# Kernel optimization log

Measured on AMD Instinct MI355X. Metric: run time of the kernel, lower is better.

## Reference

```python
import jax, jax.numpy as jnp
import numpy as np

N_NODES = 50000
N_EDGES = 800000
IN_DIM = 128
EDGE_DIM = 16
HIDDEN = 128
N_LAYERS = 3
N_GRAPHS = 256
BN_EPS = 1e-5


def setup_inputs() -> dict:
    key = jax.random.key(0)
    ks = jax.random.split(key, 24)
    s = 0.05
    inp = {
        "x": jax.random.normal(ks[0], (N_NODES, IN_DIM), jnp.float32),
        "edge_index": jax.random.randint(ks[1], (2, N_EDGES), 0, N_NODES, jnp.int32),
        "edge_attr": jax.random.normal(ks[2], (N_EDGES, EDGE_DIM), jnp.float32),
        "batch": jnp.sort(jax.random.randint(ks[3], (N_NODES,), 0, N_GRAPHS, jnp.int32)),
        "n_graphs": N_GRAPHS,
        # input projection
        "lin_in_w": jax.random.normal(ks[4], (IN_DIM, HIDDEN), jnp.float32) * s,
        "lin_in_b": jnp.zeros((HIDDEN,), jnp.float32),
        # per-layer message MLP (stacked over layers)
        "msg_w1": jax.random.normal(ks[5], (N_LAYERS, HIDDEN + EDGE_DIM, HIDDEN), jnp.float32) * s,
        "msg_b1": jnp.zeros((N_LAYERS, HIDDEN), jnp.float32),
        "msg_w2": jax.random.normal(ks[6], (N_LAYERS, HIDDEN, HIDDEN), jnp.float32) * s,
        "msg_b2": jnp.zeros((N_LAYERS, HIDDEN), jnp.float32),
        # BatchNorm (eval mode: running stats)
        "bn_gamma": jnp.ones((N_LAYERS, HIDDEN), jnp.float32),
        "bn_beta": jnp.zeros((N_LAYERS, HIDDEN), jnp.float32),
        "bn_mean": jax.random.normal(ks[7], (N_LAYERS, HIDDEN), jnp.float32) * 0.01,
        "bn_var": jax.random.uniform(ks[8], (N_LAYERS, HIDDEN), jnp.float32, 0.5, 1.5),
        # GRUCell params (PyTorch layout: [3*H, H], gate order r,z,n)
        "gru_wih": jax.random.normal(ks[9], (N_LAYERS, 3 * HIDDEN, HIDDEN), jnp.float32) * s,
        "gru_whh": jax.random.normal(ks[10], (N_LAYERS, 3 * HIDDEN, HIDDEN), jnp.float32) * s,
        "gru_bih": jnp.zeros((N_LAYERS, 3 * HIDDEN), jnp.float32),
        "gru_bhh": jnp.zeros((N_LAYERS, 3 * HIDDEN), jnp.float32),
        # readout linear: [2H -> H]
        "ro_w": jax.random.normal(ks[11], (2 * HIDDEN, HIDDEN), jnp.float32) * s,
        "ro_b": jnp.zeros((HIDDEN,), jnp.float32),
    }
    return inp


def _gru_cell(x, h, wih, whh, bih, bhh):
    gi = x @ wih.T + bih  # [N, 3H]
    gh = h @ whh.T + bhh
    ir, iz, inn = jnp.split(gi, 3, axis=1)
    hr, hz, hn = jnp.split(gh, 3, axis=1)
    r = jax.nn.sigmoid(ir + hr)
    z = jax.nn.sigmoid(iz + hz)
    n = jnp.tanh(inn + r * hn)
    return (1.0 - z) * n + z * h


def reference(x, edge_index, edge_attr, batch, n_graphs,
              lin_in_w, lin_in_b, msg_w1, msg_b1, msg_w2, msg_b2,
              bn_gamma, bn_beta, bn_mean, bn_var,
              gru_wih, gru_whh, gru_bih, gru_bhh, ro_w, ro_b):
    h = jax.nn.relu(x @ lin_in_w + lin_in_b)  # [N, H]
    src, dst = edge_index[0], edge_index[1]
    n_nodes = h.shape[0]
    for l in range(N_LAYERS):
        m_in = jnp.concatenate([h[src], edge_attr], axis=1)  # [E, H+Ed]
        m = jax.nn.relu(m_in @ msg_w1[l] + msg_b1[l]) @ msg_w2[l] + msg_b2[l]  # [E, H]
        agg = jax.ops.segment_sum(m, dst, num_segments=n_nodes)  # scatter-add
        h_new = _gru_cell(agg, h, gru_wih[l], gru_whh[l], gru_bih[l], gru_bhh[l])
        bn = (h_new - bn_mean[l]) * jax.lax.rsqrt(bn_var[l] + BN_EPS) * bn_gamma[l] + bn_beta[l]
        h = h + bn  # dropout is identity in eval mode
    # readout: segment mean + segment max over graphs
    cnt = jax.ops.segment_sum(jnp.ones((n_nodes, 1), h.dtype), batch, num_segments=n_graphs)
    z_sum = jax.ops.segment_sum(h, batch, num_segments=n_graphs)
    z_mean = z_sum / jnp.maximum(cnt, 1.0)
    z_max = jax.ops.segment_max(h, batch, num_segments=n_graphs)
    z_max = jnp.where(cnt > 0, z_max, 0.0)  # empty graphs -> 0 (as in torch code)
    z = jax.nn.relu(jnp.concatenate([z_mean, z_max], axis=1) @ ro_w + ro_b)
    return z
```

## Files before the change

kernel.cpp:

```cpp
#include <hip/hip_runtime.h>
#include <math.h>

constexpr int NN = 50000;
constexpr int NE = 800000;
constexpr int H  = 128;
constexpr int ED = 16;
constexpr int NL = 3;
constexpr int NG = 256;

typedef __attribute__((ext_vector_type(8))) short bf8;
typedef __attribute__((ext_vector_type(4))) float f32x4;

__device__ __forceinline__ unsigned short f2bf(float f) {
    unsigned u = __float_as_uint(f);
    unsigned r = (u + 0x7FFFu + ((u >> 16) & 1u)) >> 16;
    return (unsigned short)r;
}
__device__ __forceinline__ float bf2f(unsigned short b) {
    return __uint_as_float(((unsigned)b) << 16);
}

__global__ __launch_bounds__(256) void k_sort_zero(int* __restrict__ counts) {
    int i = blockIdx.x * 256 + threadIdx.x;
    counts[i] = 0;
}

__global__ __launch_bounds__(256) void k_hist(const int* __restrict__ ei,
                                              int* __restrict__ counts) {
    int e = blockIdx.x * 256 + threadIdx.x;
    if (e < NE) atomicAdd(&counts[ei[NE + e]], 1);
}

__global__ __launch_bounds__(256) void k_scan1(const int* __restrict__ counts,
                                               int* __restrict__ incl,
                                               int* __restrict__ bsum) {
    __shared__ int s[256];
    int t = threadIdx.x;
    int i = blockIdx.x * 256 + t;
    int v = counts[i];
    s[t] = v;
    __syncthreads();
    #pragma unroll
    for (int off = 1; off < 256; off <<= 1) {
        int x = (t >= off) ? s[t - off] : 0;
        __syncthreads();
        s[t] += x;
        __syncthreads();
    }
    incl[i] = s[t];
    if (t == 255) bsum[blockIdx.x] = s[255];
}

__global__ __launch_bounds__(256) void k_scan2(int* __restrict__ bsum) {
    __shared__ int s[256];
    int t = threadIdx.x;
    int v = (t < 196) ? bsum[t] : 0;
    s[t] = v;
    __syncthreads();
    #pragma unroll
    for (int off = 1; off < 256; off <<= 1) {
        int x = (t >= off) ? s[t - off] : 0;
        __syncthreads();
        s[t] += x;
        __syncthreads();
    }
    if (t < 196) bsum[t] = s[t] - v;
}

__global__ __launch_bounds__(256) void k_scan3(const int* __restrict__ counts,
                                               const int* __restrict__ incl,
                                               const int* __restrict__ bsum,
                                               int* __restrict__ cur) {
    int i = blockIdx.x * 256 + threadIdx.x;
    cur[i] = incl[i] - counts[i] + bsum[blockIdx.x];
}

__global__ __launch_bounds__(256) void k_scatter_perm(const int* __restrict__ ei,
                                                      int* __restrict__ cur,
                                                      int* __restrict__ perm) {
    int e = blockIdx.x * 256 + threadIdx.x;
    if (e < NE) {
        int d = ei[NE + e];
        int pos = atomicAdd(&cur[d], 1);
        perm[pos] = e;
    }
}

__global__ __launch_bounds__(256) void k_gather(const int* __restrict__ ei,
                                                const float* __restrict__ ea,
                                                int* __restrict__ perm,
                                                int* __restrict__ dsts,
                                                unsigned short* __restrict__ ea_bf) {
    int i = blockIdx.x * 256 + threadIdx.x;
    if (i >= NE) return;
    int e = perm[i];
    perm[i] = ei[e];
    dsts[i] = ei[NE + e];
    const float4* s = (const float4*)(ea + (size_t)e * ED);
    float4 v[4];
    #pragma unroll
    for (int j = 0; j < 4; ++j) v[j] = s[j];
    union { uint4 u[2]; unsigned short sh[16]; } pk;
    #pragma unroll
    for (int j = 0; j < 4; ++j) {
        pk.sh[j * 4 + 0] = f2bf(v[j].x); pk.sh[j * 4 + 1] = f2bf(v[j].y);
        pk.sh[j * 4 + 2] = f2bf(v[j].z); pk.sh[j * 4 + 3] = f2bf(v[j].w);
    }
    uint4* d = (uint4*)(ea_bf + (size_t)i * 16);
    d[0] = pk.u[0];
    d[1] = pk.u[1];
}

__global__ __launch_bounds__(256) void k_prep(const float* __restrict__ wih,
                                              const float* __restrict__ whh,
                                              const float* __restrict__ w1,
                                              const float* __restrict__ w2,
                                              const float* __restrict__ lin_w,
                                              unsigned short* __restrict__ wgru,
                                              unsigned short* __restrict__ w1et,
                                              unsigned short* __restrict__ w2t,
                                              unsigned short* __restrict__ w1ht,
                                              unsigned short* __restrict__ winT) {
    int i = blockIdx.x * 256 + threadIdx.x;
    if (i < 294912) {
        int m = i / 147456, rem = i % 147456;
        wgru[i] = f2bf((m == 0 ? wih : whh)[rem]);
        return;
    }
    i -= 294912;
    if (i < NL * 128 * 32) {
        int l = i / 4096, rem = i % 4096;
        int n = rem >> 5, k = rem & 31;
        float v = (k < ED) ? w1[(size_t)l * 144 * 128 + (size_t)(128 + k) * 128 + n] : 0.f;
        w1et[i] = f2bf(v);
        return;
    }
    i -= NL * 128 * 32;
    if (i < NL * 128 * 128) {
        int l = i / 16384, rem = i % 16384;
        int n = rem >> 7, k = rem & 127;
        w2t[i] = f2bf(w2[(size_t)l * 16384 + (size_t)k * 128 + n]);
        return;
    }
    i -= NL * 128 * 128;
    if (i < NL * 128 * 128) {
        int l = i / 16384, rem = i % 16384;
        int n = rem >> 7, k = rem & 127;
        w1ht[i] = f2bf(w1[(size_t)l * 144 * 128 + (size_t)k * 128 + n]);
        return;
    }
    i -= NL * 128 * 128;
    if (i < 128 * 128) {
        int n = i >> 7, k = i & 127;
        winT[i] = f2bf(lin_w[k * 128 + n]);
    }
}

template <bool RELU, bool BIAS, bool OUT_F32, bool OUT_BF>
__global__ __launch_bounds__(256) void k_mfma_gemm(const float* __restrict__ A,
                                                   const unsigned short* __restrict__ Bt,
                                                   const float* __restrict__ bias,
                                                   float* __restrict__ C_f,
                                                   unsigned short* __restrict__ C_bf,
                                                   int M) {
    __shared__ unsigned short As[32][136];
    const int t = threadIdx.x;
    const int w = t >> 6, lane = t & 63, l15 = lane & 15, q = lane >> 4;
    const int n0 = blockIdx.x * 32;

    bf8 bfr[2][4];
    #pragma unroll
    for (int nt = 0; nt < 2; ++nt) {
        int n = w * 32 + nt * 16 + l15;
        #pragma unroll
        for (int ks = 0; ks < 4; ++ks)
            bfr[nt][ks] = *(const bf8*)(Bt + (size_t)n * 128 + ks * 32 + q * 8);
    }

    {
        int r = t >> 3, cs = (t & 7) * 16;
        int row = n0 + r;
        float4 v[4];
        if (row < M) {
            const float4* src = (const float4*)(A + (size_t)row * H + cs);
            #pragma unroll
            for (int j = 0; j < 4; ++j) v[j] = src[j];
        } else {
            #pragma unroll
            for (int j = 0; j < 4; ++j) v[j] = make_float4(0.f, 0.f, 0.f, 0.f);
        }
        union { uint4 u[2]; unsigned short s[16]; } pk;
        #pragma unroll
        for (int j = 0; j < 4; ++j) {
            pk.s[j * 4 + 0] = f2bf(v[j].x); pk.s[j * 4 + 1] = f2bf(v[j].y);
            pk.s[j * 4 + 2] = f2bf(v[j].z); pk.s[j * 4 + 3] = f2bf(v[j].w);
        }
        *(uint4*)&As[r][cs] = pk.u[0];
        *(uint4*)&As[r][cs + 8] = pk.u[1];
    }
    __syncthreads();

    f32x4 acc[2][2];
    #pragma unroll
    for (int mt = 0; mt < 2; ++mt)
        #pragma unroll
        for (int nt = 0; nt < 2; ++nt) acc[mt][nt] = {0.f, 0.f, 0.f, 0.f};

    #pragma unroll
    for (int ks = 0; ks < 4; ++ks) {
        #pragma unroll
        for (int mt = 0; mt < 2; ++mt) {
            bf8 af = *(const bf8*)&As[mt * 16 + l15][ks * 32 + q * 8];
            acc[mt][0] = __builtin_amdgcn_mfma_f32_16x16x32_bf16(af, bfr[0][ks], acc[mt][0], 0, 0, 0);
            acc[mt][1] = __builtin_amdgcn_mfma_f32_16x16x32_bf16(af, bfr[1][ks], acc[mt][1], 0, 0, 0);
        }
    }

    #pragma unroll
    for (int nt = 0; nt < 2; ++nt) {
        int col = w * 32 + nt * 16 + l15;
        float bv = BIAS ? bias[col] : 0.f;
        #pragma unroll
        for (int mt = 0; mt < 2; ++mt) {
            #pragma unroll
            for (int r = 0; r < 4; ++r) {
                int node = n0 + mt * 16 + q * 4 + r;
                if (node < M) {
                    float v = acc[mt][nt][r] + bv;
                    if (RELU) v = fmaxf(v, 0.f);
                    if (OUT_F32) C_f[(size_t)node * H + col] = v;
                    if (OUT_BF)  C_bf[(size_t)node * H + col] = f2bf(v);
                }
            }
        }
    }
}

__global__ __launch_bounds__(256, 6) void k_edge_mfma(
        const unsigned short* __restrict__ p,
        const int* __restrict__ srcs,
        const int* __restrict__ dsts,
        const unsigned short* __restrict__ ea_bf,
        const unsigned short* __restrict__ w1et,
        const float* __restrict__ b1,
        const unsigned short* __restrict__ w2t,
        const float* __restrict__ b2,
        float* __restrict__ agg) {
    __shared__ unsigned short u_s[64][136];
    __shared__ int src_s[64], dst_s[64];

    const int t    = threadIdx.x;
    const int w    = t >> 6;
    const int lane = t & 63;
    const int l15  = lane & 15;
    const int q    = lane >> 4;

    bf8 w1f[2];
    bf8 w2f[2][4];
    float b1v[2], b2v[2];
    #pragma unroll
    for (int nt = 0; nt < 2; ++nt) {
        int n = w * 32 + nt * 16 + l15;
        w1f[nt] = *(const bf8*)(w1et + (size_t)n * 32 + q * 8);
        #pragma unroll
        for (int ks = 0; ks < 4; ++ks)
            w2f[nt][ks] = *(const bf8*)(w2t + (size_t)n * 128 + ks * 32 + q * 8);
        b1v[nt] = b1[n];
        b2v[nt] = b2[n];
    }

    const f32x4 zero = {0.f, 0.f, 0.f, 0.f};

    for (int base = blockIdx.x * 64; base < NE; base += gridDim.x * 64) {
        if (t < 64)       src_s[t] = srcs[base + t];
        else if (t < 128) dst_s[t - 64] = dsts[base + t - 64];
        __syncthreads();

        {
            int row = t >> 4, seg = t & 15;
            #pragma unroll
            for (int it = 0; it < 4; ++it) {
                int rr = row + 16 * it;
                *(uint4*)&u_s[rr][seg * 8] =
                    *(const uint4*)(p + (size_t)src_s[rr] * H + seg * 8);
            }
        }

        f32x4 acc1[4][2];
        #pragma unroll
        for (int mt = 0; mt < 4; ++mt) {
            bf8 af = {0, 0, 0, 0, 0, 0, 0, 0};
            if (q < 2)
                af = *(const bf8*)(ea_bf + (size_t)(base + mt * 16 + l15) * 16 + q * 8);
            #pragma unroll
            for (int nt = 0; nt < 2; ++nt)
                acc1[mt][nt] = __builtin_amdgcn_mfma_f32_16x16x32_bf16(af, w1f[nt], zero, 0, 0, 0);
        }
        __syncthreads();

        #pragma unroll
        for (int mt = 0; mt < 4; ++mt) {
            #pragma unroll
            for (int r = 0; r < 4; ++r) {
                int er = mt * 16 + q * 4 + r;
                #pragma unroll
                for (int nt = 0; nt < 2; ++nt) {
                    int col = w * 32 + nt * 16 + l15;
                    float v = acc1[mt][nt][r] + bf2f(u_s[er][col]) + b1v[nt];
                    u_s[er][col] = f2bf(fmaxf(v, 0.f));
                }
            }
        }
        __syncthreads();

        f32x4 acc2[4][2];
        #pragma unroll
        for (int mt = 0; mt < 4; ++mt)
            #pragma unroll
            for (int nt = 0; nt < 2; ++nt) acc2[mt][nt] = zero;

        #pragma unroll
        for (int ks = 0; ks < 4; ++ks) {
            #pragma unroll
            for (int mt = 0; mt < 4; ++mt) {
                bf8 af = *(const bf8*)&u_s[mt * 16 + l15][ks * 32 + q * 8];
                acc2[mt][0] = __builtin_amdgcn_mfma_f32_16x16x32_bf16(af, w2f[0][ks], acc2[mt][0], 0, 0, 0);
                acc2[mt][1] = __builtin_amdgcn_mfma_f32_16x16x32_bf16(af, w2f[1][ks], acc2[mt][1], 0, 0, 0);
            }
        }
        __syncthreads();

        #pragma unroll
        for (int mt = 0; mt < 4; ++mt) {
            #pragma unroll
            for (int r = 0; r < 4; ++r) {
                int er = mt * 16 + q * 4 + r;
                #pragma unroll
                for (int nt = 0; nt < 2; ++nt) {
                    int col = w * 32 + nt * 16 + l15;
                    u_s[er][col] = f2bf(acc2[mt][nt][r] + b2v[nt]);
                }
            }
        }
        __syncthreads();

        {
            int c = t & 127, hh = t >> 7;
            float sum = 0.f;
            int prev = dst_s[hh * 32];
            #pragma unroll 4
            for (int i = 0; i < 32; ++i) {
                int e = hh * 32 + i;
                int d = dst_s[e];
                float v = bf2f(u_s[e][c]);
                if (d != prev) {
                    atomicAdd(&agg[(size_t)prev * H + c], sum);
                    sum = 0.f;
                    prev = d;
                }
                sum += v;
            }
            atomicAdd(&agg[(size_t)prev * H + c], sum);
        }
        __syncthreads();
    }
}

__device__ __forceinline__ float sigmoidf_(float x) { return 1.f / (1.f + expf(-x)); }

__global__ __launch_bounds__(256) void k_gru_mfma(const float* __restrict__ agg,
                                                  float* __restrict__ h,
                                                  const unsigned short* __restrict__ wih,
                                                  const unsigned short* __restrict__ whh,
                                                  const float* __restrict__ bih,
                                                  const float* __restrict__ bhh,
                                                  const float* __restrict__ gamma,
                                                  const float* __restrict__ beta,
                                                  const float* __restrict__ mean,
                                                  const float* __restrict__ var) {
    __shared__ unsigned short ab[32][136];
    __shared__ unsigned short hb[32][136];
    __shared__ float hf[32][132];
    const int t = threadIdx.x;
    const int w = t >> 6, lane = t & 63, l15 = lane & 15, q = lane >> 4;
    const int n0 = blockIdx.x * 32;

    {
        int r = t >> 3, cs = (t & 7) * 16;
        int row = n0 + r;
        float4 va[4], vh[4];
        if (row < NN) {
            const float4* sa = (const float4*)(agg + (size_t)row * H + cs);
            const float4* sh = (const float4*)(h + (size_t)row * H + cs);
            #pragma unroll
            for (int j = 0; j < 4; ++j) { va[j] = sa[j]; vh[j] = sh[j]; }
        } else {
            #pragma unroll
            for (int j = 0; j < 4; ++j) {
                va[j] = make_float4(0.f, 0.f, 0.f, 0.f);
                vh[j] = va[j];
            }
        }
        union { uint4 u[2]; unsigned short s[16]; } pa, ph;
        #pragma unroll
        for (int j = 0; j < 4; ++j) {
            pa.s[j * 4 + 0] = f2bf(va[j].x); pa.s[j * 4 + 1] = f2bf(va[j].y);
            pa.s[j * 4 + 2] = f2bf(va[j].z); pa.s[j * 4 + 3] = f2bf(va[j].w);
            ph.s[j * 4 + 0] = f2bf(vh[j].x); ph.s[j * 4 + 1] = f2bf(vh[j].y);
            ph.s[j * 4 + 2] = f2bf(vh[j].z); ph.s[j * 4 + 3] = f2bf(vh[j].w);
            *(float4*)&hf[r][cs + j * 4] = vh[j];
        }
        *(uint4*)&ab[r][cs] = pa.u[0];  *(uint4*)&ab[r][cs + 8] = pa.u[1];
        *(uint4*)&hb[r][cs] = ph.u[0];  *(uint4*)&hb[r][cs + 8] = ph.u[1];
    }
    __syncthreads();

    f32x4 acc[2][2][3][2];
    #pragma unroll
    for (int mt = 0; mt < 2; ++mt)
        #pragma unroll
        for (int io = 0; io < 2; ++io)
            #pragma unroll
            for (int g = 0; g < 3; ++g)
                #pragma unroll
                for (int nt = 0; nt < 2; ++nt) acc[mt][io][g][nt] = {0.f, 0.f, 0.f, 0.f};

    #pragma unroll
    for (int ks = 0; ks < 4; ++ks) {
        bf8 a_a[2], a_h[2];
        #pragma unroll
        for (int mt = 0; mt < 2; ++mt) {
            a_a[mt] = *(const bf8*)&ab[mt * 16 + l15][ks * 32 + q * 8];
            a_h[mt] = *(const bf8*)&hb[mt * 16 + l15][ks * 32 + q * 8];
        }
        #pragma unroll
        for (int g = 0; g < 3; ++g) {
            #pragma unroll
            for (int nt = 0; nt < 2; ++nt) {
                int n = g * 128 + w * 32 + nt * 16 + l15;
                bf8 bi = *(const bf8*)(wih + (size_t)n * 128 + ks * 32 + q * 8);
                bf8 bh = *(const bf8*)(whh + (size_t)n * 128 + ks * 32 + q * 8);
                #pragma unroll
                for (int mt = 0; mt < 2; ++mt) {
                    acc[mt][0][g][nt] = __builtin_amdgcn_mfma_f32_16x16x32_bf16(a_a[mt], bi, acc[mt][0][g][nt], 0, 0, 0);
                    acc[mt][1][g][nt] = __builtin_amdgcn_mfma_f32_16x16x32_bf16(a_h[mt], bh, acc[mt][1][g][nt], 0, 0, 0);
                }
            }
        }
    }

    #pragma unroll
    for (int nt = 0; nt < 2; ++nt) {
        int col = w * 32 + nt * 16 + l15;
        float bir = bih[col], biz = bih[128 + col], bin = bih[256 + col];
        float bhr = bhh[col], bhz = bhh[128 + col], bhn = bhh[256 + col];
        float ga = gamma[col], be = beta[col], mu = mean[col];
        float iv = rsqrtf(var[col] + 1e-5f);
        #pragma unroll
        for (int mt = 0; mt < 2; ++mt) {
            #pragma unroll
            for (int r = 0; r < 4; ++r) {
                int nl = mt * 16 + q * 4 + r;
                int node = n0 + nl;
                if (node < NN) {
                    float ir = acc[mt][0][0][nt][r] + bir;
                    float iz = acc[mt][0][1][nt][r] + biz;
                    float in = acc[mt][0][2][nt][r] + bin;
                    float hr = acc[mt][1][0][nt][r] + bhr;
                    float hz = acc[mt][1][1][nt][r] + bhz;
                    float hn = acc[mt][1][2][nt][r] + bhn;
                    float rg = sigmoidf_(ir + hr);
                    float zg = sigmoidf_(iz + hz);
                    float ng = tanhf(in + rg * hn);
                    float hv = hf[nl][col];
                    float hnew = (1.f - zg) * ng + zg * hv;
                    float bn = (hnew - mu) * iv * ga + be;
                    h[(size_t)node * H + col] = hv + bn;
                }
            }
        }
    }
}

__device__ __forceinline__ unsigned fkey(float f) {
    unsigned b = __float_as_uint(f);
    return (b & 0x80000000u) ? ~b : (b | 0x80000000u);
}
__device__ __forceinline__ float funkey(unsigned k) {
    unsigned b = (k & 0x80000000u) ? (k & 0x7FFFFFFFu) : ~k;
    return __uint_as_float(b);
}

__global__ __launch_bounds__(256) void k_ro_scan(const float* __restrict__ h,
                                                 const int* __restrict__ batch,
                                                 float* __restrict__ gsum,
                                                 unsigned* __restrict__ gmaxb,
                                                 float* __restrict__ gcnt) {
    __shared__ int bt_s[64];
    const int t = threadIdx.x;
    const int n0 = blockIdx.x * 64;
    if (t < 64) bt_s[t] = (n0 + t < NN) ? batch[n0 + t] : -1;
    __syncthreads();

    int c = t & 127, hh = t >> 7;
    float sum = 0.f, mx = -3.4e38f, cnt = 0.f;
    int prev = bt_s[hh * 32];
    #pragma unroll 4
    for (int i = 0; i < 32; ++i) {
        int e = hh * 32 + i;
        int g = bt_s[e];
        if (g != prev) {
            if (prev >= 0) {
                atomicAdd(&gsum[prev * H + c], sum);
                atomicMax(&gmaxb[prev * H + c], fkey(mx));
                if (c == 0) atomicAdd(&gcnt[prev], cnt);
            }
            sum = 0.f; mx = -3.4e38f; cnt = 0.f;
            prev = g;
        }
        if (g >= 0) {
            float v = h[(size_t)(n0 + e) * H + c];
            sum += v;
            mx = fmaxf(mx, v);
            cnt += 1.f;
        }
    }
    if (prev >= 0) {
        atomicAdd(&gsum[prev * H + c], sum);
        atomicMax(&gmaxb[prev * H + c], fkey(mx));
        if (c == 0) atomicAdd(&gcnt[prev], cnt);
    }
}

__global__ __launch_bounds__(128) void k_ro_final(const float* __restrict__ gsum,
                                                  const unsigned* __restrict__ gmaxb,
                                                  const float* __restrict__ gcnt,
                                                  const float* __restrict__ row,
                                                  const float* __restrict__ rob,
                                                  float* __restrict__ out) {
    __shared__ float cat[256];
    const int g = blockIdx.x, t = threadIdx.x;
    float cnt = gcnt[g];
    float inv = 1.f / fmaxf(cnt, 1.f);
    cat[t] = gsum[g * H + t] * inv;
    float mx = funkey(gmaxb[g * H + t]);
    cat[128 + t] = (cnt > 0.f) ? mx : 0.f;
    __syncthreads();
    float acc = rob[t];
    #pragma unroll 4
    for (int k = 0; k < 256; ++k) acc += cat[k] * row[k * H + t];
    out[g * H + t] = fmaxf(acc, 0.f);
}

extern "C" void kernel_launch(void* const* d_in, const int* in_sizes, int n_in,
                              void* d_out, int out_size, void* d_ws, size_t ws_size,
                              hipStream_t stream) {
    const float* x        = (const float*)d_in[0];
    const int*   ei       = (const int*)d_in[1];
    const float* ea       = (const float*)d_in[2];
    const int*   batch    = (const int*)d_in[3];
    const float* lin_in_w = (const float*)d_in[5];
    const float* lin_in_b = (const float*)d_in[6];
    const float* msg_w1   = (const float*)d_in[7];
    const float* msg_b1   = (const float*)d_in[8];
    const float* msg_w2   = (const float*)d_in[9];
    const float* msg_b2   = (const float*)d_in[10];
    const float* bn_gamma = (const float*)d_in[11];
    const float* bn_beta  = (const float*)d_in[12];
    const float* bn_mean  = (const float*)d_in[13];
    const float* bn_var   = (const float*)d_in[14];
    const float* gru_wih  = (const float*)d_in[15];
    const float* gru_whh  = (const float*)d_in[16];
    const float* gru_bih  = (const float*)d_in[17];
    const float* gru_bhh  = (const float*)d_in[18];
    const float* ro_w     = (const float*)d_in[19];
    const float* ro_b     = (const float*)d_in[20];

    float* ws = (float*)d_ws;
    float*          h     = ws;
    float*          agg   = ws + 6400000;
    unsigned short* p_bf  = (unsigned short*)(ws + 12800000);
    float*          gsum  = ws + 16000000;
    unsigned*       gmaxb = (unsigned*)(ws + 16032768);
    float*          gcnt  = ws + 16065536;
    unsigned short* wgru  = (unsigned short*)(ws + 16065792);
    unsigned short* w1et  = (unsigned short*)(ws + 16213248);
    unsigned short* w2t   = (unsigned short*)(ws + 16219392);
    unsigned short* w1ht  = (unsigned short*)(ws + 16243968);
    unsigned short* winT  = (unsigned short*)(ws + 16268544);
    int*            cnts  = (int*)(ws + 16276736);
    int*            incl  = (int*)(ws + 16326912);
    int*            cur   = (int*)(ws + 16377088);
    int*            bsum  = (int*)(ws + 16427264);
    int*            srcs  = (int*)(ws + 16427520);
    int*            dsts  = (int*)(ws + 17227520);
    unsigned short* ea_bf = (unsigned short*)(ws + 18027520);

    k_prep<<<1648, 256, 0, stream>>>(gru_wih, gru_whh, msg_w1, msg_w2, lin_in_w,
                                     wgru, w1et, w2t, w1ht, winT);

    k_sort_zero<<<196, 256, 0, stream>>>(cnts);
    k_hist<<<3125, 256, 0, stream>>>(ei, cnts);
    k_scan1<<<196, 256, 0, stream>>>(cnts, incl, bsum);
    k_scan2<<<1, 256, 0, stream>>>(bsum);
    k_scan3<<<196, 256, 0, stream>>>(cnts, incl, bsum, cur);
    k_scatter_perm<<<3125, 256, 0, stream>>>(ei, cur, srcs);
    k_gather<<<3125, 256, 0, stream>>>(ei, ea, srcs, dsts, ea_bf);

    k_mfma_gemm<true, true, true, false><<<1563, 256, 0, stream>>>(
        x, winT, lin_in_b, h, nullptr, NN);

    for (int l = 0; l < NL; ++l) {
        k_mfma_gemm<false, false, false, true><<<1563, 256, 0, stream>>>(
            h, w1ht + (size_t)l * 16384, nullptr, nullptr, p_bf, NN);
        hipMemsetAsync(agg, 0, (size_t)NN * H * sizeof(float), stream);
        k_edge_mfma<<<1536, 256, 0, stream>>>(p_bf, srcs, dsts, ea_bf,
                                              w1et + (size_t)l * 4096, msg_b1 + l * 128,
                                              w2t + (size_t)l * 16384, msg_b2 + l * 128,
                                              agg);
        k_gru_mfma<<<1563, 256, 0, stream>>>(agg, h,
                                             wgru + (size_t)l * 49152,
                                             wgru + (size_t)(NL + l) * 49152,
                                             gru_bih + l * 384, gru_bhh + l * 384,
                                             bn_gamma + l * 128, bn_beta + l * 128,
                                             bn_mean + l * 128, bn_var + l * 128);
    }

    hipMemsetAsync(gsum, 0, (size_t)(NG * H * 2 + NG) * sizeof(float), stream);
    k_ro_scan<<<782, 256, 0, stream>>>(h, batch, gsum, gmaxb, gcnt);
    k_ro_final<<<NG, 128, 0, stream>>>(gsum, gmaxb, gcnt, ro_w, ro_b, (float*)d_out);
}
```

Baseline: 964.7 us.

## Fuse per-layer node projection into input-proj and GRU kernels; replace memsets

The h@W1h projection GEMM that produced p_bf is folded into the epilogue of the input projection and of the previous layer's GRU kernel, which reuse the fresh h tile held in LDS. This removes one kernel launch per layer and a full re-read of h from memory. The hipMemsetAsync calls are replaced by small zeroing kernels, and the edge kernel grid and occupancy hint change from 1536 blocks with launch bounds 6 to 1024 blocks with launch bounds 4. The cost is extra register pressure and LDS syncs in the GRU kernel.

```diff
diff --git a/kernel.cpp b/kernel.cpp
--- a/kernel.cpp
+++ b/kernel.cpp
@@ -18,6 +18,11 @@
 }
 __device__ __forceinline__ float bf2f(unsigned short b) {
     return __uint_as_float(((unsigned)b) << 16);
+}
+
+__global__ __launch_bounds__(256) void k_zero4(float4* __restrict__ a, int n4) {
+    int i = blockIdx.x * 256 + threadIdx.x;
+    if (i < n4) a[i] = make_float4(0.f, 0.f, 0.f, 0.f);
 }
 
 __global__ __launch_bounds__(256) void k_sort_zero(int* __restrict__ counts) {
@@ -156,13 +161,12 @@
     }
 }
 
-template <bool RELU, bool BIAS, bool OUT_F32, bool OUT_BF>
-__global__ __launch_bounds__(256) void k_mfma_gemm(const float* __restrict__ A,
-                                                   const unsigned short* __restrict__ Bt,
-                                                   const float* __restrict__ bias,
-                                                   float* __restrict__ C_f,
-                                                   unsigned short* __restrict__ C_bf,
-                                                   int M) {
+__global__ __launch_bounds__(256) void k_inproj(const float* __restrict__ x,
+                                                const unsigned short* __restrict__ winT,
+                                                const float* __restrict__ bias,
+                                                const unsigned short* __restrict__ w1h0,
+                                                float* __restrict__ h,
+                                                unsigned short* __restrict__ p_bf) {
     __shared__ unsigned short As[32][136];
     const int t = threadIdx.x;
     const int w = t >> 6, lane = t & 63, l15 = lane & 15, q = lane >> 4;
@@ -174,15 +178,15 @@
         int n = w * 32 + nt * 16 + l15;
         #pragma unroll
         for (int ks = 0; ks < 4; ++ks)
-            bfr[nt][ks] = *(const bf8*)(Bt + (size_t)n * 128 + ks * 32 + q * 8);
+            bfr[nt][ks] = *(const bf8*)(winT + (size_t)n * 128 + ks * 32 + q * 8);
     }
 
     {
         int r = t >> 3, cs = (t & 7) * 16;
         int row = n0 + r;
         float4 v[4];
-        if (row < M) {
-            const float4* src = (const float4*)(A + (size_t)row * H + cs);
+        if (row < NN) {
+            const float4* src = (const float4*)(x + (size_t)row * H + cs);
             #pragma unroll
             for (int j = 0; j < 4; ++j) v[j] = src[j];
         } else {
@@ -215,28 +219,63 @@
             acc[mt][1] = __builtin_amdgcn_mfma_f32_16x16x32_bf16(af, bfr[1][ks], acc[mt][1], 0, 0, 0);
         }
     }
+    __syncthreads();
 
     #pragma unroll
     for (int nt = 0; nt < 2; ++nt) {
         int col = w * 32 + nt * 16 + l15;
-        float bv = BIAS ? bias[col] : 0.f;
+        float bv = bias[col];
+        #pragma unroll
+        for (int mt = 0; mt < 2; ++mt) {
+            #pragma unroll
+            for (int r = 0; r < 4; ++r) {
+                int nl = mt * 16 + q * 4 + r;
+                int node = n0 + nl;
+                float v = fmaxf(acc[mt][nt][r] + bv, 0.f);
+                if (node < NN) h[(size_t)node * H + col] = v;
+                As[nl][col] = f2bf(v);
+            }
+        }
+    }
+    __syncthreads();
+
+    bf8 pfr[2][4];
+    #pragma unroll
+    for (int nt = 0; nt < 2; ++nt) {
+        int n = w * 32 + nt * 16 + l15;
+        #pragma unroll
+        for (int ks = 0; ks < 4; ++ks)
+            pfr[nt][ks] = *(const bf8*)(w1h0 + (size_t)n * 128 + ks * 32 + q * 8);
+    }
+    f32x4 accp[2][2];
+    #pragma unroll
+    for (int mt = 0; mt < 2; ++mt)
+        #pragma unroll
+        for (int nt = 0; nt < 2; ++nt) accp[mt][nt] = {0.f, 0.f, 0.f, 0.f};
+    #pragma unroll
+    for (int ks = 0; ks < 4; ++ks) {
+        #pragma unroll
+        for (int mt = 0; mt < 2; ++mt) {
+            bf8 af = *(const bf8*)&As[mt * 16 + l15][ks * 32 + q * 8];
+            accp[mt][0] = __builtin_amdgcn_mfma_f32_16x16x32_bf16(af, pfr[0][ks], accp[mt][0], 0, 0, 0);
+            accp[mt][1] = __builtin_amdgcn_mfma_f32_16x16x32_bf16(af, pfr[1][ks], accp[mt][1], 0, 0, 0);
+        }
+    }
+    #pragma unroll
+    for (int nt = 0; nt < 2; ++nt) {
+        int col = w * 32 + nt * 16 + l15;
         #pragma unroll
         for (int mt = 0; mt < 2; ++mt) {
             #pragma unroll
             for (int r = 0; r < 4; ++r) {
                 int node = n0 + mt * 16 + q * 4 + r;
-                if (node < M) {
-                    float v = acc[mt][nt][r] + bv;
-                    if (RELU) v = fmaxf(v, 0.f);
-                    if (OUT_F32) C_f[(size_t)node * H + col] = v;
-                    if (OUT_BF)  C_bf[(size_t)node * H + col] = f2bf(v);
-                }
-            }
-        }
-    }
-}
-
-__global__ __launch_bounds__(256, 6) void k_edge_mfma(
+                if (node < NN) p_bf[(size_t)node * H + col] = f2bf(accp[mt][nt][r]);
+            }
+        }
+    }
+}
+
+__global__ __launch_bounds__(256, 4) void k_edge_mfma(
         const unsigned short* __restrict__ p,
         const int* __restrict__ srcs,
         const int* __restrict__ dsts,
@@ -377,7 +416,9 @@
                                                   const float* __restrict__ gamma,
                                                   const float* __restrict__ beta,
                                                   const float* __restrict__ mean,
-                                                  const float* __restrict__ var) {
+                                                  const float* __restrict__ var,
+                                                  const unsigned short* __restrict__ w1h_next,
+                                                  unsigned short* __restrict__ p_bf) {
     __shared__ unsigned short ab[32][136];
     __shared__ unsigned short hb[32][136];
     __shared__ float hf[32][132];
@@ -449,6 +490,7 @@
         }
     }
 
+    float rout[2][2][4];
     #pragma unroll
     for (int nt = 0; nt < 2; ++nt) {
         int col = w * 32 + nt * 16 + l15;
@@ -462,20 +504,67 @@
             for (int r = 0; r < 4; ++r) {
                 int nl = mt * 16 + q * 4 + r;
                 int node = n0 + nl;
-                if (node < NN) {
-                    float ir = acc[mt][0][0][nt][r] + bir;
-                    float iz = acc[mt][0][1][nt][r] + biz;
-                    float in = acc[mt][0][2][nt][r] + bin;
-                    float hr = acc[mt][1][0][nt][r] + bhr;
-                    float hz = acc[mt][1][1][nt][r] + bhz;
-                    float hn = acc[mt][1][2][nt][r] + bhn;
-                    float rg = sigmoidf_(ir + hr);
-                    float zg = sigmoidf_(iz + hz);
-                    float ng = tanhf(in + rg * hn);
-                    float hv = hf[nl][col];
-                    float hnew = (1.f - zg) * ng + zg * hv;
-                    float bn = (hnew - mu) * iv * ga + be;
-                    h[(size_t)node * H + col] = hv + bn;
+                float ir = acc[mt][0][0][nt][r] + bir;
+                float iz = acc[mt][0][1][nt][r] + biz;
+                float in = acc[mt][0][2][nt][r] + bin;
+                float hr = acc[mt][1][0][nt][r] + bhr;
+                float hz = acc[mt][1][1][nt][r] + bhz;
+                float hn = acc[mt][1][2][nt][r] + bhn;
+                float rg = sigmoidf_(ir + hr);
+                float zg = sigmoidf_(iz + hz);
+                float ng = tanhf(in + rg * hn);
+                float hv = hf[nl][col];
+                float hnew = (1.f - zg) * ng + zg * hv;
+                float bn = (hnew - mu) * iv * ga + be;
+                float out = hv + bn;
+                rout[nt][mt][r] = out;
+                if (node < NN) h[(size_t)node * H + col] = out;
+            }
+        }
+    }
+
+    if (w1h_next != nullptr) {
+        __syncthreads();
+        #pragma unroll
+        for (int nt = 0; nt < 2; ++nt) {
+            int col = w * 32 + nt * 16 + l15;
+            #pragma unroll
+            for (int mt = 0; mt < 2; ++mt)
+                #pragma unroll
+                for (int r = 0; r < 4; ++r)
+                    hb[mt * 16 + q * 4 + r][col] = f2bf(rout[nt][mt][r]);
+        }
+        __syncthreads();
+
+        f32x4 accp[2][2];
+        #pragma unroll
+        for (int mt = 0; mt < 2; ++mt)
+            #pragma unroll
+            for (int nt = 0; nt < 2; ++nt) accp[mt][nt] = {0.f, 0.f, 0.f, 0.f};
+        #pragma unroll
+        for (int ks = 0; ks < 4; ++ks) {
+            bf8 pf0, pf1;
+            {
+                int n = w * 32 + l15;
+                pf0 = *(const bf8*)(w1h_next + (size_t)n * 128 + ks * 32 + q * 8);
+                pf1 = *(const bf8*)(w1h_next + (size_t)(n + 16) * 128 + ks * 32 + q * 8);
+            }
+            #pragma unroll
+            for (int mt = 0; mt < 2; ++mt) {
+                bf8 af = *(const bf8*)&hb[mt * 16 + l15][ks * 32 + q * 8];
+                accp[mt][0] = __builtin_amdgcn_mfma_f32_16x16x32_bf16(af, pf0, accp[mt][0], 0, 0, 0);
+                accp[mt][1] = __builtin_amdgcn_mfma_f32_16x16x32_bf16(af, pf1, accp[mt][1], 0, 0, 0);
+            }
+        }
+        #pragma unroll
+        for (int nt = 0; nt < 2; ++nt) {
+            int col = w * 32 + nt * 16 + l15;
+            #pragma unroll
+            for (int mt = 0; mt < 2; ++mt) {
+                #pragma unroll
+                for (int r = 0; r < 4; ++r) {
+                    int node = n0 + mt * 16 + q * 4 + r;
+                    if (node < NN) p_bf[(size_t)node * H + col] = f2bf(accp[mt][nt][r]);
                 }
             }
         }
@@ -489,6 +578,14 @@
 __device__ __forceinline__ float funkey(unsigned k) {
     unsigned b = (k & 0x80000000u) ? (k & 0x7FFFFFFFu) : ~k;
     return __uint_as_float(b);
+}
+
+__global__ __launch_bounds__(256) void k_ro_init(float* __restrict__ gsum,
+                                                 unsigned* __restrict__ gmaxb,
+                                                 float* __restrict__ gcnt) {
+    int i = blockIdx.x * 256 + threadIdx.x;
+    if (i < NG * H) { gsum[i] = 0.f; gmaxb[i] = 0u; }
+    if (i < NG) gcnt[i] = 0.f;
 }
 
 __global__ __launch_bounds__(256) void k_ro_scan(const float* __restrict__ h,
@@ -607,26 +704,25 @@
     k_scatter_perm<<<3125, 256, 0, stream>>>(ei, cur, srcs);
     k_gather<<<3125, 256, 0, stream>>>(ei, ea, srcs, dsts, ea_bf);
 
-    k_mfma_gemm<true, true, true, false><<<1563, 256, 0, stream>>>(
-        x, winT, lin_in_b, h, nullptr, NN);
+    k_inproj<<<1563, 256, 0, stream>>>(x, winT, lin_in_b, w1ht, h, p_bf);
 
     for (int l = 0; l < NL; ++l) {
-        k_mfma_gemm<false, false, false, true><<<1563, 256, 0, stream>>>(
-            h, w1ht + (size_t)l * 16384, nullptr, nullptr, p_bf, NN);
-        hipMemsetAsync(agg, 0, (size_t)NN * H * sizeof(float), stream);
-        k_edge_mfma<<<1536, 256, 0, stream>>>(p_bf, srcs, dsts, ea_bf,
+        k_zero4<<<6250, 256, 0, stream>>>((float4*)agg, 1600000);
+        k_edge_mfma<<<1024, 256, 0, stream>>>(p_bf, srcs, dsts, ea_bf,
                                               w1et + (size_t)l * 4096, msg_b1 + l * 128,
                                               w2t + (size_t)l * 16384, msg_b2 + l * 128,
                                               agg);
+        const unsigned short* w1h_next = (l + 1 < NL) ? (w1ht + (size_t)(l + 1) * 16384) : nullptr;
         k_gru_mfma<<<1563, 256, 0, stream>>>(agg, h,
                                              wgru + (size_t)l * 49152,
                                              wgru + (size_t)(NL + l) * 49152,
                                              gru_bih + l * 384, gru_bhh + l * 384,
                                              bn_gamma + l * 128, bn_beta + l * 128,
-                                             bn_mean + l * 128, bn_var + l * 128);
-    }
-
-    hipMemsetAsync(gsum, 0, (size_t)(NG * H * 2 + NG) * sizeof(float), stream);
+                                             bn_mean + l * 128, bn_var + l * 128,
+                                             w1h_next, p_bf);
+    }
+
+    k_ro_init<<<128, 256, 0, stream>>>(gsum, gmaxb, gcnt);
     k_ro_scan<<<782, 256, 0, stream>>>(h, batch, gsum, gmaxb, gcnt);
     k_ro_final<<<NG, 128, 0, stream>>>(gsum, gmaxb, gcnt, ro_w, ro_b, (float*)d_out);
 }
```

Result: faster. 849.6 us (-11.9%).
